# Kernel tuning notes

Measured on AMD Instinct MI355X. Metric: run time of the kernel, lower is better.

The kernel has to match this reference:

```python
import jax, jax.numpy as jnp
import numpy as np

K = 3
OUT_H, OUT_W = 32, 512
INVALID_DIST = 1e10  # stands in for filtering out zero points on the reference side


def _downsample(pc, out_H=OUT_H, out_W=OUT_W):
    # pc: [B, H, W, 3] -> [B, out_H, out_W, 3] via strided index selection
    B, H, W, _ = pc.shape
    sH, sW = H // out_H, W // out_W
    return pc[:, : out_H * sH : sH, : out_W * sW : sW, :]


def _batch_knn_mean(tgt, src):
    # tgt: [Nt, 3] reference points; src: [Ns, 3] query points.
    # move_zero_point filters points whose xyz are all zero; with fixed shapes we
    # emulate this by masking: invalid refs get huge distance (never selected in
    # top-k unless all refs invalid), invalid queries are excluded from the mean.
    valid_t = jnp.any(tgt != 0.0, axis=-1)  # [Nt]
    valid_s = jnp.any(src != 0.0, axis=-1)  # [Ns]
    # pairwise squared Euclidean distance [Ns, Nt]
    d2 = (
        jnp.sum(src * src, axis=-1)[:, None]
        + jnp.sum(tgt * tgt, axis=-1)[None, :]
        - 2.0 * (src @ tgt.T)
    )
    d = jnp.sqrt(jnp.maximum(d2, 0.0))  # KNN_CUDA returns Euclidean distance
    d = jnp.where(valid_t[None, :], d, INVALID_DIST)
    neg_topk, _ = jax.lax.top_k(-d, K)  # k smallest distances per query
    dk = -neg_topk  # [Ns, K]
    w = valid_s.astype(d.dtype)
    denom = K * jnp.maximum(jnp.sum(w), 1.0)
    return jnp.sum(dk * w[:, None]) / denom  # mean over valid query knn dists


def reference(source_pc, target_pc):
    # source_pc: [B, H, W, 3]; target_pc: [B, 3, H, W]
    B = source_pc.shape[0]
    tgt = _downsample(jnp.transpose(target_pc, (0, 2, 3, 1))).reshape(B, -1, 3)
    src = _downsample(source_pc).reshape(B, -1, 3)
    per_batch = jax.vmap(_batch_knn_mean)(tgt, src)  # [B]
    return jnp.mean(per_batch)


def setup_inputs() -> dict:
    key = jax.random.key(0)
    k1, k2 = jax.random.split(key)
    source_pc = jax.random.normal(k1, (2, 64, 2048, 3), dtype=jnp.float32)
    target_pc = jax.random.normal(k2, (2, 3, 64, 2048), dtype=jnp.float32)
    return {"source_pc": source_pc, "target_pc": target_pc}
```

## Files before the change

kernel.cpp:

```cpp
#include <hip/hip_runtime.h>
#include <math.h>

#define NB 2
#define NQ 16384
#define IN_H 64
#define IN_W 2048
#define BIG 1e30f
#define NQT (NB * NQ)

typedef __bf16 bf16x8 __attribute__((ext_vector_type(8)));
typedef float f32x16 __attribute__((ext_vector_type(16)));

__device__ inline float med3(float a, float b, float c) {
    return __builtin_amdgcn_fmed3f(a, b, c);
}
#define INSERT3(B0, B1, B2, V)                    \
    do { float _v = (V);                          \
         (B2) = med3((B1), (B2), _v);             \
         (B1) = med3((B0), (B1), _v);             \
         (B0) = fminf((B0), _v); } while (0)

union PK { __bf16 h[8]; uint4 u; };

__global__ __launch_bounds__(256) void pack_kernel(
    const float* __restrict__ tgt_pc,
    uint4* __restrict__ packed,
    float4* __restrict__ tgt4,
    float* __restrict__ zws)
{
    if (blockIdx.x == 0 && threadIdx.x < 16) zws[threadIdx.x] = 0.f;

    int gid = blockIdx.x * 256 + threadIdx.x;
    int b = gid >> 14, t = gid & (NQ - 1);
    int oh = t >> 9, ow = t & 511;
    const size_t PL = (size_t)IN_H * IN_W;
    size_t base = ((size_t)(b * 3) * IN_H + oh * 2) * IN_W + ow * 4;
    float x = tgt_pc[base], y = tgt_pc[base + PL], z = tgt_pc[base + 2 * PL];
    bool valid = (x != 0.f) || (y != 0.f) || (z != 0.f);
    float ntx = x * x + y * y + z * z;
    float nt = valid ? ntx : BIG;
    float tx = valid ? -2.f * x : 0.f;
    float ty = valid ? -2.f * y : 0.f;
    float tz = valid ? -2.f * z : 0.f;

    __bf16 txh = (__bf16)tx, tyh = (__bf16)ty, tzh = (__bf16)tz;
    __bf16 txl = (__bf16)(tx - (float)txh);
    __bf16 tyl = (__bf16)(ty - (float)tyh);
    __bf16 tzl = (__bf16)(tz - (float)tzh);
    __bf16 nth = (__bf16)nt;
    __bf16 ntl = (__bf16)(nt - (float)nth);

    PK h0, h1;
    h0.h[0] = txh; h0.h[1] = tyh; h0.h[2] = tzh; h0.h[3] = txh;
    h0.h[4] = tyh; h0.h[5] = tzh; h0.h[6] = txl; h0.h[7] = tyl;
    h1.h[0] = tzl; h1.h[1] = nth; h1.h[2] = ntl; h1.h[3] = (__bf16)1.0f;
    h1.h[4] = (__bf16)1.0f; h1.h[5] = (__bf16)0.0f;
    h1.h[6] = (__bf16)0.0f; h1.h[7] = (__bf16)0.0f;

    int tile = t >> 5, m = t & 31;
    size_t o = (size_t)(b * 512 + tile) * 64 + m;
    packed[o]      = h0.u;
    packed[o + 32] = h1.u;

    tgt4[gid] = make_float4(valid ? x : 0.f, valid ? y : 0.f,
                            valid ? z : 0.f, valid ? ntx : 1e20f);
}

__global__ __launch_bounds__(256, 4) void knn_mfma(
    const float* __restrict__ src_pc,
    const uint4* __restrict__ packed,
    const float4* __restrict__ tgt4,
    float* __restrict__ partial)
{
    __shared__ uint4 lds[2][1024];
    const int tid = threadIdx.x;
    const int lane = tid & 63;
    const int w = tid >> 6;
    int blk = blockIdx.x;
    int qt = blk & 127;
    int quarter = (blk >> 7) & 3;
    int b = blk >> 9;

    int n = lane & 31;
    int q = qt * 128 + w * 32 + n;
    size_t sbase = (((size_t)b * IN_H + (q >> 9) * 2) * IN_W + (q & 511) * 4) * 3;
    float sx = src_pc[sbase], sy = src_pc[sbase + 1], sz = src_pc[sbase + 2];
    float ns = sx * sx + sy * sy + sz * sz;
    __bf16 sxh = (__bf16)sx, syh = (__bf16)sy, szh = (__bf16)sz;
    __bf16 sxl = (__bf16)(sx - (float)sxh);
    __bf16 syl = (__bf16)(sy - (float)syh);
    __bf16 szl = (__bf16)(sz - (float)szh);
    __bf16 nsh = (__bf16)ns;
    __bf16 nsl = (__bf16)(ns - (float)nsh);
    bf16x8 bq;
    if ((lane >> 5) == 0) {
        bq[0] = sxh; bq[1] = syh; bq[2] = szh; bq[3] = sxl;
        bq[4] = syl; bq[5] = szl; bq[6] = sxh; bq[7] = syh;
    } else {
        bq[0] = szh; bq[1] = (__bf16)1.0f; bq[2] = (__bf16)1.0f; bq[3] = nsh;
        bq[4] = nsl; bq[5] = (__bf16)0.0f; bq[6] = (__bf16)0.0f; bq[7] = (__bf16)0.0f;
    }

    f32x16 zero;
    #pragma unroll
    for (int i = 0; i < 16; ++i) zero[i] = 0.f;

    float c0 = BIG, c1 = BIG, c2 = BIG;

    const uint4* pkq = packed + (size_t)b * 32768 + (size_t)quarter * 8192;

    uint4 r[4];
    #pragma unroll
    for (int i = 0; i < 4; ++i) r[i] = pkq[tid + 256 * i];
    #pragma unroll
    for (int i = 0; i < 4; ++i) lds[0][tid + 256 * i] = r[i];
    __syncthreads();

    for (int c = 0; c < 8; ++c) {
        int cur = c & 1;
        uint4 rn[4];
        if (c < 7) {
            const uint4* s = pkq + (c + 1) * 1024;
            #pragma unroll
            for (int i = 0; i < 4; ++i) rn[i] = s[tid + 256 * i];
        }
        const uint4* buf = lds[cur];
        #pragma unroll 2
        for (int t = 0; t < 16; ++t) {
            bf16x8 af = __builtin_bit_cast(bf16x8, buf[t * 64 + lane]);
            f32x16 d = __builtin_amdgcn_mfma_f32_32x32x16_bf16(af, bq, zero, 0, 0, 0);
            float m0 = fminf(fminf(d[0], d[1]), fminf(d[2], d[3]));
            float m1 = fminf(fminf(d[4], d[5]), fminf(d[6], d[7]));
            float m2 = fminf(fminf(d[8], d[9]), fminf(d[10], d[11]));
            float m3 = fminf(fminf(d[12], d[13]), fminf(d[14], d[15]));
            float m = fminf(fminf(m0, m1), fminf(m2, m3));
            unsigned u = (__float_as_uint(m) & ~127u) | (unsigned)(c * 16 + t);
            float pv = __uint_as_float(u);
            INSERT3(c0, c1, c2, pv);
        }
        if (c < 7) {
            #pragma unroll
            for (int i = 0; i < 4; ++i) lds[1 - cur][tid + 256 * i] = rn[i];
        }
        __syncthreads();
    }

    int half = lane >> 5;
    int ti[3] = { (int)(__float_as_uint(c0) & 127u),
                  (int)(__float_as_uint(c1) & 127u),
                  (int)(__float_as_uint(c2) & 127u) };
    float e0 = BIG, e1 = BIG, e2 = BIG;
    const float4* t4b = tgt4 + (size_t)b * NQ + (size_t)quarter * 4096;
    #pragma unroll
    for (int i = 0; i < 3; ++i) {
        int tbase = ti[i] * 32 + 4 * half;
        #pragma unroll
        for (int rr = 0; rr < 16; ++rr) {
            int row = (rr & 3) + 8 * (rr >> 2);
            float4 t4 = t4b[tbase + row];
            float dot = sx * t4.x;
            dot = fmaf(sy, t4.y, dot);
            dot = fmaf(sz, t4.z, dot);
            float d2 = fmaf(-2.f, dot, ns + t4.w);
            INSERT3(e0, e1, e2, d2);
        }
    }

    float f0 = __shfl_down(e0, 32, 64);
    float f1 = __shfl_down(e1, 32, 64);
    float f2 = __shfl_down(e2, 32, 64);
    if (lane < 32) {
        INSERT3(e0, e1, e2, f0);
        INSERT3(e0, e1, e2, f1);
        INSERT3(e0, e1, e2, f2);
        int gq = b * NQ + q;
        partial[(quarter * 3 + 0) * NQT + gq] = e0;
        partial[(quarter * 3 + 1) * NQT + gq] = e1;
        partial[(quarter * 3 + 2) * NQT + gq] = e2;
    }
}

__global__ __launch_bounds__(256) void merge_final(
    const float* __restrict__ partial,
    const float* __restrict__ src_pc,
    float* __restrict__ accum,
    int* __restrict__ done_cnt,
    float* __restrict__ out)
{
    int gid = blockIdx.x * 256 + threadIdx.x;
    int b = gid >> 14;
    int q = gid & (NQ - 1);

    float b0 = BIG, b1 = BIG, b2 = BIG;
    #pragma unroll
    for (int c = 0; c < 12; ++c) {
        float v = partial[c * NQT + gid];
        INSERT3(b0, b1, b2, v);
    }

    size_t base = (((size_t)b * IN_H + (q >> 9) * 2) * IN_W + (q & 511) * 4) * 3;
    float x = src_pc[base], y = src_pc[base + 1], z = src_pc[base + 2];
    float wt = ((x != 0.f) || (y != 0.f) || (z != 0.f)) ? 1.f : 0.f;

    float d = fminf(sqrtf(fmaxf(b0, 0.f)), 1e10f)
            + fminf(sqrtf(fmaxf(b1, 0.f)), 1e10f)
            + fminf(sqrtf(fmaxf(b2, 0.f)), 1e10f);
    float dsum = d * wt;

    #pragma unroll
    for (int off = 32; off > 0; off >>= 1) {
        dsum += __shfl_down(dsum, off, 64);
        wt   += __shfl_down(wt, off, 64);
    }
    __shared__ float sd[4], sw4[4];
    int lane = threadIdx.x & 63, wv = threadIdx.x >> 6;
    if (lane == 0) { sd[wv] = dsum; sw4[wv] = wt; }
    __syncthreads();
    if (threadIdx.x == 0) {
        atomicAdd(&accum[b * 2 + 0], sd[0] + sd[1] + sd[2] + sd[3]);
        atomicAdd(&accum[b * 2 + 1], sw4[0] + sw4[1] + sw4[2] + sw4[3]);
        __threadfence();
        int done = atomicAdd(done_cnt, 1);
        if (done == (int)gridDim.x - 1) {
            float s0 = atomicAdd(&accum[0], 0.f);
            float c0 = atomicAdd(&accum[1], 0.f);
            float s1 = atomicAdd(&accum[2], 0.f);
            float c1 = atomicAdd(&accum[3], 0.f);
            float r = s0 / (3.0f * fmaxf(c0, 1.0f))
                    + s1 / (3.0f * fmaxf(c1, 1.0f));
            out[0] = r / (float)NB;
        }
    }
}

extern "C" void kernel_launch(void* const* d_in, const int* in_sizes, int n_in,
                              void* d_out, int out_size, void* d_ws, size_t ws_size,
                              hipStream_t stream) {
    const float* src_pc = (const float*)d_in[0];
    const float* tgt_pc = (const float*)d_in[1];
    float* out = (float*)d_out;

    char* ws = (char*)d_ws;
    float*  accum   = (float*)ws;
    int*    done    = (int*)(ws + 32);
    float*  partial = (float*)(ws + 64);
    uint4*  packed  = (uint4*)(ws + 2097152);
    float4* tgt4    = (float4*)(ws + 3145728);

    pack_kernel<<<NQT / 256, 256, 0, stream>>>(tgt_pc, packed, tgt4, (float*)ws);
    knn_mfma<<<NB * 4 * 128, 256, 0, stream>>>(src_pc, packed, tgt4, partial);
    merge_final<<<NQT / 256, 256, 0, stream>>>(partial, src_pc, accum, done, out);
}
```

Baseline: 119.9 us.

## Stream target tiles directly from global into registers, drop LDS staging

Removes the shared-memory double buffer and block-wide barriers in the KNN MFMA kernel. Each wave now loads packed target tiles straight from global/L2 into register double buffers of eight tiles, fully unrolled. Two independent top-3 accumulators alternate by tile parity to shorten the med3 dependency chain, and are merged at the end. This trades LDS traffic and syncs for redundant per-wave global loads (four waves read the same data) and higher register pressure.

```diff
diff --git a/kernel.cpp b/kernel.cpp
--- a/kernel.cpp
+++ b/kernel.cpp
@@ -7,6 +7,8 @@
 #define IN_W 2048
 #define BIG 1e30f
 #define NQT (NB * NQ)
+#define NG 4
+#define NP (NG * 3)
 
 typedef __bf16 bf16x8 __attribute__((ext_vector_type(8)));
 typedef float f32x16 __attribute__((ext_vector_type(16)));
@@ -66,13 +68,27 @@
                             valid ? z : 0.f, valid ? ntx : 1e20f);
 }
 
+#define COMPUTE_TILE(U, IDX)                                                  \
+    do {                                                                      \
+        bf16x8 af = __builtin_bit_cast(bf16x8, (U));                          \
+        f32x16 d = __builtin_amdgcn_mfma_f32_32x32x16_bf16(af, bq, zero, 0, 0, 0); \
+        float m0 = fminf(fminf(d[0], d[1]), fminf(d[2], d[3]));               \
+        float m1 = fminf(fminf(d[4], d[5]), fminf(d[6], d[7]));               \
+        float m2 = fminf(fminf(d[8], d[9]), fminf(d[10], d[11]));             \
+        float m3 = fminf(fminf(d[12], d[13]), fminf(d[14], d[15]));           \
+        float m = fminf(fminf(m0, m1), fminf(m2, m3));                        \
+        unsigned u = (__float_as_uint(m) & ~127u) | (unsigned)(IDX);          \
+        float pv = __uint_as_float(u);                                        \
+        if ((IDX) & 1) { INSERT3(c0b, c1b, c2b, pv); }                        \
+        else           { INSERT3(c0a, c1a, c2a, pv); }                        \
+    } while (0)
+
 __global__ __launch_bounds__(256, 4) void knn_mfma(
     const float* __restrict__ src_pc,
     const uint4* __restrict__ packed,
     const float4* __restrict__ tgt4,
     float* __restrict__ partial)
 {
-    __shared__ uint4 lds[2][1024];
     const int tid = threadIdx.x;
     const int lane = tid & 63;
     const int w = tid >> 6;
@@ -105,50 +121,37 @@
     #pragma unroll
     for (int i = 0; i < 16; ++i) zero[i] = 0.f;
 
-    float c0 = BIG, c1 = BIG, c2 = BIG;
-
-    const uint4* pkq = packed + (size_t)b * 32768 + (size_t)quarter * 8192;
-
-    uint4 r[4];
-    #pragma unroll
-    for (int i = 0; i < 4; ++i) r[i] = pkq[tid + 256 * i];
-    #pragma unroll
-    for (int i = 0; i < 4; ++i) lds[0][tid + 256 * i] = r[i];
-    __syncthreads();
-
-    for (int c = 0; c < 8; ++c) {
-        int cur = c & 1;
-        uint4 rn[4];
-        if (c < 7) {
-            const uint4* s = pkq + (c + 1) * 1024;
+    float c0a = BIG, c1a = BIG, c2a = BIG;
+    float c0b = BIG, c1b = BIG, c2b = BIG;
+
+    const uint4* pkq = packed + (size_t)b * 32768 + (size_t)quarter * 8192 + lane;
+
+    uint4 bufA[8], bufB[8];
+    #pragma unroll
+    for (int i = 0; i < 8; ++i) bufA[i] = pkq[i * 64];
+
+    #pragma unroll
+    for (int gg = 0; gg < 8; ++gg) {
+        #pragma unroll
+        for (int i = 0; i < 8; ++i) bufB[i] = pkq[((2 * gg + 1) * 8 + i) * 64];
+        #pragma unroll
+        for (int i = 0; i < 8; ++i) COMPUTE_TILE(bufA[i], 2 * gg * 8 + i);
+        if (gg < 7) {
             #pragma unroll
-            for (int i = 0; i < 4; ++i) rn[i] = s[tid + 256 * i];
+            for (int i = 0; i < 8; ++i) bufA[i] = pkq[((2 * gg + 2) * 8 + i) * 64];
         }
-        const uint4* buf = lds[cur];
-        #pragma unroll 2
-        for (int t = 0; t < 16; ++t) {
-            bf16x8 af = __builtin_bit_cast(bf16x8, buf[t * 64 + lane]);
-            f32x16 d = __builtin_amdgcn_mfma_f32_32x32x16_bf16(af, bq, zero, 0, 0, 0);
-            float m0 = fminf(fminf(d[0], d[1]), fminf(d[2], d[3]));
-            float m1 = fminf(fminf(d[4], d[5]), fminf(d[6], d[7]));
-            float m2 = fminf(fminf(d[8], d[9]), fminf(d[10], d[11]));
-            float m3 = fminf(fminf(d[12], d[13]), fminf(d[14], d[15]));
-            float m = fminf(fminf(m0, m1), fminf(m2, m3));
-            unsigned u = (__float_as_uint(m) & ~127u) | (unsigned)(c * 16 + t);
-            float pv = __uint_as_float(u);
-            INSERT3(c0, c1, c2, pv);
-        }
-        if (c < 7) {
-            #pragma unroll
-            for (int i = 0; i < 4; ++i) lds[1 - cur][tid + 256 * i] = rn[i];
-        }
-        __syncthreads();
-    }
+        #pragma unroll
+        for (int i = 0; i < 8; ++i) COMPUTE_TILE(bufB[i], (2 * gg + 1) * 8 + i);
+    }
+
+    INSERT3(c0a, c1a, c2a, c0b);
+    INSERT3(c0a, c1a, c2a, c1b);
+    INSERT3(c0a, c1a, c2a, c2b);
 
     int half = lane >> 5;
-    int ti[3] = { (int)(__float_as_uint(c0) & 127u),
-                  (int)(__float_as_uint(c1) & 127u),
-                  (int)(__float_as_uint(c2) & 127u) };
+    int ti[3] = { (int)(__float_as_uint(c0a) & 127u),
+                  (int)(__float_as_uint(c1a) & 127u),
+                  (int)(__float_as_uint(c2a) & 127u) };
     float e0 = BIG, e1 = BIG, e2 = BIG;
     const float4* t4b = tgt4 + (size_t)b * NQ + (size_t)quarter * 4096;
     #pragma unroll
@@ -193,7 +196,7 @@
 
     float b0 = BIG, b1 = BIG, b2 = BIG;
     #pragma unroll
-    for (int c = 0; c < 12; ++c) {
+    for (int c = 0; c < NP; ++c) {
         float v = partial[c * NQT + gid];
         INSERT3(b0, b1, b2, v);
     }
@@ -248,6 +251,6 @@
     float4* tgt4    = (float4*)(ws + 3145728);
 
     pack_kernel<<<NQT / 256, 256, 0, stream>>>(tgt_pc, packed, tgt4, (float*)ws);
-    knn_mfma<<<NB * 4 * 128, 256, 0, stream>>>(src_pc, packed, tgt4, partial);
+    knn_mfma<<<NB * NG * 128, 256, 0, stream>>>(src_pc, packed, tgt4, partial);
     merge_final<<<NQT / 256, 256, 0, stream>>>(partial, src_pc, accum, done, out);
 }
```

New measurement: 108.4 us. 9.6% less time.
